# Kernel tuning notes

Measured on AMD Instinct MI355X. Metric: run time of the kernel, lower is better.

Reference implementation:

```python
import jax, jax.numpy as jnp
import numpy as np

B, S, D, H = 4, 2048, 2048, 16
DH = D // H


def setup_inputs() -> dict:
    key = jax.random.key(0)
    ks = jax.random.split(key, 11)
    p = 0.02  # keep pre-softmax logits in a sane range
    return {
        "x": jax.random.normal(ks[0], (B, S, D), jnp.float32),
        "Wq": jax.random.normal(ks[1], (D, D), jnp.float32) * p,
        "bq": jax.random.normal(ks[2], (D,), jnp.float32) * p,
        "Wk": jax.random.normal(ks[3], (D, D), jnp.float32) * p,
        "bk": jax.random.normal(ks[4], (D,), jnp.float32) * p,
        "Wv": jax.random.normal(ks[5], (D, D), jnp.float32) * p,
        "bv": jax.random.normal(ks[6], (D,), jnp.float32) * p,
        "Wo": jax.random.normal(ks[7], (D, D), jnp.float32) * p,
        "bo": jax.random.normal(ks[8], (D,), jnp.float32) * p,
        "spiral_weight": jax.random.normal(ks[9], (H,), jnp.float32),
        "helix_rotation": jax.random.normal(ks[10], (D,), jnp.float32),
    }


def reference(x, Wq, bq, Wk, bk, Wv, bv, Wo, bo, spiral_weight, helix_rotation):
    b, s, d = x.shape
    h, dh = H, d // H
    # projections (torch Linear: x @ W.T + b), split into heads
    q = (x @ Wq.T + bq).reshape(b, s, h, dh)
    k = (x @ Wk.T + bk).reshape(b, s, h, dh)
    v = (x @ Wv.T + bv).reshape(b, s, h, dh)
    # cos/sin helix gating, applied per (head, head_dim) channel
    rot = helix_rotation.reshape(h, dh)
    q = q * jnp.cos(rot)
    k = k * jnp.sin(rot)
    # per-head scaled scores: [b,h,s,s]
    scores = jnp.einsum("bshd,bthd->bhst", q, k) / np.sqrt(dh).astype(np.float32)
    scores = scores * spiral_weight[None, :, None, None]
    attn = jax.nn.softmax(scores, axis=-1)
    out = jnp.einsum("bhst,bthd->bshd", attn, v).reshape(b, s, d)
    return out @ Wo.T + bo
```

## Files before the change

kernel.cpp:

```cpp
#include <hip/hip_runtime.h>
#include <math.h>

#define B_ 4
#define S_ 2048
#define D_ 2048
#define H_ 16
#define DH_ 128

typedef unsigned short u16;
typedef unsigned int u32;
typedef u16 u16x8 __attribute__((ext_vector_type(8)));
typedef __bf16 bf16x8 __attribute__((ext_vector_type(8)));
typedef float f32x4 __attribute__((ext_vector_type(4)));

__device__ inline u16 f2bf(float f) {
    unsigned int u = __builtin_bit_cast(unsigned int, f);
    unsigned int lsb = (u >> 16) & 1u;
    u += 0x7fffu + lsb;
    return (u16)(u >> 16);
}

__device__ inline f32x4 mfma16(u16x8 a, u16x8 b, f32x4 c) {
    return __builtin_amdgcn_mfma_f32_16x16x32_bf16(
        __builtin_bit_cast(bf16x8, a), __builtin_bit_cast(bf16x8, b), c, 0, 0, 0);
}

__device__ inline void gl2lds16(const u16* g, u16* l) {
    __builtin_amdgcn_global_load_lds(
        (const __attribute__((address_space(1))) void*)g,
        (__attribute__((address_space(3))) void*)l, 16, 0, 0);
}

__device__ inline void block_barrier() {
    asm volatile("" ::: "memory");
    __builtin_amdgcn_s_barrier();
    asm volatile("" ::: "memory");
}

__global__ __launch_bounds__(256) void cvt_f32_bf16(const float* __restrict__ src,
                                                    u16* __restrict__ dst, int n8) {
    int i = blockIdx.x * 256 + threadIdx.x;
    if (i >= n8) return;
    const float4* s = (const float4*)src + (size_t)i * 2;
    float4 a = s[0], b = s[1];
    u16x8 o;
    o[0] = f2bf(a.x); o[1] = f2bf(a.y); o[2] = f2bf(a.z); o[3] = f2bf(a.w);
    o[4] = f2bf(b.x); o[5] = f2bf(b.y); o[6] = f2bf(b.z); o[7] = f2bf(b.w);
    *((u16x8*)dst + i) = o;
}

__global__ __launch_bounds__(256) void cvt4_f32_bf16(const float* __restrict__ s0,
                                                     const float* __restrict__ s1,
                                                     const float* __restrict__ s2,
                                                     const float* __restrict__ s3,
                                                     u16* __restrict__ dst) {
    const int region = blockIdx.x >> 11;
    const int i = (blockIdx.x & 2047) * 256 + threadIdx.x;
    const float* src = region == 0 ? s0 : region == 1 ? s1 : region == 2 ? s2 : s3;
    const float4* s = (const float4*)src + (size_t)i * 2;
    float4 a = s[0], b = s[1];
    u16x8 o;
    o[0] = f2bf(a.x); o[1] = f2bf(a.y); o[2] = f2bf(a.z); o[3] = f2bf(a.w);
    o[4] = f2bf(b.x); o[5] = f2bf(b.y); o[6] = f2bf(b.z); o[7] = f2bf(b.w);
    *((u16x8*)dst + (size_t)region * 524288 + i) = o;
}

template <int VOUT, typename OutT>
__device__ __forceinline__ void gemm_core(const u16* __restrict__ A,
                                          const u16* __restrict__ Bw,
                                          const float* __restrict__ bias,
                                          const float* __restrict__ helix,
                                          OutT* __restrict__ C,
                                          int M, int N, int K,
                                          int tm, int tn, int gate) {
    __shared__ __align__(16) u16 As[2][256 * 64];
    __shared__ __align__(16) u16 Bs[2][256 * 64];

    const int tid = threadIdx.x;
    const int lane = tid & 63, w = tid >> 6;
    const int lr = lane & 15, quad = lane >> 4;
    const int wm = w & 1, wn = w >> 1;
    const int NT = K >> 6;

    const u16* Asrc = A + (size_t)(tm * 256) * K;
    const u16* Bsrc = Bw + (size_t)(tn * 256) * K;

    u32 go[4][2];
    u32 lo[4][2];
#pragma unroll
    for (int q = 0; q < 2; ++q) {
        const int seg = w * 2 + q;
        const int i0 = seg * 8 + (lane >> 3);
        const int s0 = seg * 8;
        int row = (i0 & 63) | ((i0 >> 6) << 7);
        int rb = (s0 & 63) | ((s0 >> 6) << 7);
        go[0][q] = (u32)row * K + (((lane & 7) ^ (row & 7)) << 3);
        lo[0][q] = rb << 6;
        row += 64; rb += 64;
        go[3][q] = (u32)row * K + (((lane & 7) ^ (row & 7)) << 3);
        lo[3][q] = rb << 6;
        row = (i0 & 31) | ((i0 >> 5) << 6);
        rb = (s0 & 31) | ((s0 >> 5) << 6);
        go[1][q] = (u32)row * K + (((lane & 7) ^ (row & 7)) << 3);
        lo[1][q] = rb << 6;
        row += 32; rb += 32;
        go[2][q] = (u32)row * K + (((lane & 7) ^ (row & 7)) << 3);
        lo[2][q] = rb << 6;
    }

#define STAGE(u, tt)                                                          \
    do {                                                                      \
        const int kt_ = (((tt) < NT) ? (tt) : (NT - 1)) << 6;                 \
        const u16* gb_ = ((u) == 1 || (u) == 2) ? Bsrc : Asrc;                \
        u16* lb_ = ((u) == 1 || (u) == 2) ? Bs[(tt) & 1] : As[(tt) & 1];      \
        gl2lds16(gb_ + go[u][0] + kt_, lb_ + lo[u][0]);                       \
        gl2lds16(gb_ + go[u][1] + kt_, lb_ + lo[u][1]);                       \
    } while (0)

    const int koff0 = (quad * 8) ^ ((lr & 7) * 8);
    const int koff1 = (32 + quad * 8) ^ ((lr & 7) * 8);
    const int rA = wm * 128 + lr;
    const int rB = wn * 64 + lr;

    f32x4 zero = {0.f, 0.f, 0.f, 0.f};
    f32x4 acc[8][4];
#pragma unroll
    for (int im = 0; im < 8; ++im)
#pragma unroll
        for (int jn = 0; jn < 4; ++jn) acc[im][jn] = zero;

    u16x8 af[4][2], bf[4][2];

    STAGE(0, 0); STAGE(1, 0); STAGE(2, 0); STAGE(3, 0);
    STAGE(0, 1); STAGE(1, 1); STAGE(2, 1);
    asm volatile("s_waitcnt vmcnt(6)" ::: "memory");
    block_barrier();

    for (int t = 0; t < NT; ++t) {
        const u16* Ab = As[t & 1];
        const u16* Bb = Bs[t & 1];

#pragma unroll
        for (int im = 0; im < 4; ++im) {
            af[im][0] = *(const u16x8*)&Ab[(rA + im * 16) * 64 + koff0];
            af[im][1] = *(const u16x8*)&Ab[(rA + im * 16) * 64 + koff1];
        }
#pragma unroll
        for (int jn = 0; jn < 2; ++jn) {
            bf[jn][0] = *(const u16x8*)&Bb[(rB + jn * 16) * 64 + koff0];
            bf[jn][1] = *(const u16x8*)&Bb[(rB + jn * 16) * 64 + koff1];
        }
        STAGE(3, t + 1);
        block_barrier();
        asm volatile("s_waitcnt lgkmcnt(0)" ::: "memory");
        __builtin_amdgcn_s_setprio(1);
#pragma unroll
        for (int s = 0; s < 2; ++s)
#pragma unroll
            for (int im = 0; im < 4; ++im)
#pragma unroll
                for (int jn = 0; jn < 2; ++jn)
                    acc[im][jn] = mfma16(af[im][s], bf[jn][s], acc[im][jn]);
        __builtin_amdgcn_s_setprio(0);
        block_barrier();

#pragma unroll
        for (int jn = 2; jn < 4; ++jn) {
            bf[jn][0] = *(const u16x8*)&Bb[(rB + jn * 16) * 64 + koff0];
            bf[jn][1] = *(const u16x8*)&Bb[(rB + jn * 16) * 64 + koff1];
        }
        STAGE(0, t + 2);
        block_barrier();
        asm volatile("s_waitcnt lgkmcnt(0)" ::: "memory");
        __builtin_amdgcn_s_setprio(1);
#pragma unroll
        for (int s = 0; s < 2; ++s)
#pragma unroll
            for (int im = 0; im < 4; ++im)
#pragma unroll
                for (int jn = 2; jn < 4; ++jn)
                    acc[im][jn] = mfma16(af[im][s], bf[jn][s], acc[im][jn]);
        __builtin_amdgcn_s_setprio(0);
        block_barrier();

#pragma unroll
        for (int im = 0; im < 4; ++im) {
            af[im][0] = *(const u16x8*)&Ab[(rA + 64 + im * 16) * 64 + koff0];
            af[im][1] = *(const u16x8*)&Ab[(rA + 64 + im * 16) * 64 + koff1];
        }
        STAGE(1, t + 2);
        block_barrier();
        asm volatile("s_waitcnt lgkmcnt(0)" ::: "memory");
        __builtin_amdgcn_s_setprio(1);
#pragma unroll
        for (int s = 0; s < 2; ++s)
#pragma unroll
            for (int im = 0; im < 4; ++im)
#pragma unroll
                for (int jn = 0; jn < 2; ++jn)
                    acc[im + 4][jn] = mfma16(af[im][s], bf[jn][s], acc[im + 4][jn]);
        __builtin_amdgcn_s_setprio(0);
        block_barrier();

        STAGE(2, t + 2);
        asm volatile("s_waitcnt vmcnt(6)" ::: "memory");
        block_barrier();
        __builtin_amdgcn_s_setprio(1);
#pragma unroll
        for (int s = 0; s < 2; ++s)
#pragma unroll
            for (int im = 0; im < 4; ++im)
#pragma unroll
                for (int jn = 2; jn < 4; ++jn)
                    acc[im + 4][jn] = mfma16(af[im][s], bf[jn][s], acc[im + 4][jn]);
        __builtin_amdgcn_s_setprio(0);
        block_barrier();
    }
    asm volatile("s_waitcnt vmcnt(0)" ::: "memory");
#undef STAGE

    if constexpr (VOUT) {
#pragma unroll
        for (int im = 0; im < 8; ++im)
#pragma unroll
            for (int r = 0; r < 4; ++r) {
                int row = tm * 256 + wm * 128 + im * 16 + quad * 4 + r;
                float bs = bias[row];
#pragma unroll
                for (int jn = 0; jn < 4; ++jn) {
                    int col = tn * 256 + wn * 64 + jn * 16 + lr;
                    float val = acc[im][jn][r] + bs;
                    ((u16*)C)[(size_t)(col >> 11) * ((size_t)D_ * S_) +
                              (size_t)row * S_ + (col & (S_ - 1))] = f2bf(val);
                }
            }
    } else {
#pragma unroll
        for (int jn = 0; jn < 4; ++jn) {
            int col = tn * 256 + wn * 64 + jn * 16 + lr;
            float bs = bias[col];
            float g = 1.0f;
            if (gate == 1) g = cosf(helix[col]);
            if (gate == 2) g = sinf(helix[col]);
#pragma unroll
            for (int im = 0; im < 8; ++im)
#pragma unroll
                for (int r = 0; r < 4; ++r) {
                    int row = tm * 256 + wm * 128 + im * 16 + quad * 4 + r;
                    float val = (acc[im][jn][r] + bs) * g;
                    if constexpr (sizeof(OutT) == 2)
                        ((u16*)C)[(size_t)row * N + col] = f2bf(val);
                    else
                        ((float*)C)[(size_t)row * N + col] = val;
                }
        }
    }
}

template <int VOUT, typename OutT>
__global__ __launch_bounds__(512, 2) void gemm256(const u16* __restrict__ A,
                                                  const u16* __restrict__ Bw,
                                                  const float* __restrict__ bias,
                                                  const float* __restrict__ helix,
                                                  OutT* __restrict__ C,
                                                  int M, int N, int K, int gate) {
    gemm_core<VOUT, OutT>(A, Bw, bias, helix, C, M, N, K, blockIdx.y, blockIdx.x, gate);
}

__global__ __launch_bounds__(512, 2) void gemm256_qk(const u16* __restrict__ A,
                                                     const u16* __restrict__ Wq,
                                                     const u16* __restrict__ Wk,
                                                     const float* __restrict__ bq,
                                                     const float* __restrict__ bk,
                                                     const float* __restrict__ helix,
                                                     u16* __restrict__ Cq,
                                                     u16* __restrict__ Ck,
                                                     int M, int N, int K) {
    const int sel = blockIdx.x >> 3;
    const int tn = blockIdx.x & 7;
    gemm_core<0, u16>(A, sel ? Wk : Wq, sel ? bk : bq, helix, sel ? Ck : Cq,
                      M, N, K, blockIdx.y, tn, 1 + sel);
}

__global__ __launch_bounds__(256, 2) void helix_attn(const u16* __restrict__ Q,
                                                     const u16* __restrict__ Kq,
                                                     const u16* __restrict__ Vt,
                                                     const float* __restrict__ spiral,
                                                     u16* __restrict__ O) {
    __shared__ __align__(16) u16 Ks[64 * 128];
    __shared__ __align__(16) u16 Vs[128 * 72];
    __shared__ __align__(16) u16 Ps[128 * 72];

    const int tid = threadIdx.x;
    const int lane = tid & 63, w = tid >> 6;
    const int lr = lane & 15, quad = lane >> 4;

    const int bx = blockIdx.x;
    const int qt = bx & 15;
    const int h = (bx >> 4) & 15;
    const int b = bx >> 8;

    const size_t headoff = (size_t)b * S_ * D_ + (size_t)h * DH_;
    const u16* qp = Q + headoff;
    const u16* kp = Kq + headoff;
    const u16* vtp = Vt + ((size_t)b * H_ + h) * (size_t)DH_ * S_;

    const float scale2 = spiral[h] * 0.08838834764831845f * 1.4426950408889634f;

    u16x8 qf[2][4];
#pragma unroll
    for (int mb = 0; mb < 2; ++mb)
#pragma unroll
        for (int c = 0; c < 4; ++c) {
            u16x8 raw = *(const u16x8*)(qp + (size_t)(qt * 128 + mb * 64 + w * 16 + lr) * D_ +
                                        c * 32 + quad * 8);
#pragma unroll
            for (int j = 0; j < 8; ++j) {
                float f = __builtin_bit_cast(float, (u32)raw[j] << 16) * scale2;
                qf[mb][c][j] = f2bf(f);
            }
        }

    f32x4 zero = {0.f, 0.f, 0.f, 0.f};
    f32x4 Oacc[2][8];
#pragma unroll
    for (int mb = 0; mb < 2; ++mb)
#pragma unroll
        for (int n = 0; n < 8; ++n) Oacc[mb][n] = zero;
    float rs[2][4] = {{0.f, 0.f, 0.f, 0.f}, {0.f, 0.f, 0.f, 0.f}};

    const int rsw = (lr >> 1) & 7;
    const int wsw = (quad * 2) & 7;
    const int ksw = lr & 7;

    for (int tt = 0; tt < 32; ++tt) {
        const int t0 = tt * 64;
        __syncthreads();
#pragma unroll
        for (int p = 0; p < 4; ++p) {
            int lin = p * 256 + tid;
            int trow = lin >> 4;
            int kch = lin & 15;
            *(u16x8*)&Ks[trow * 128 + ((kch ^ (trow & 7)) * 8)] =
                *(const u16x8*)(kp + (size_t)(t0 + trow) * D_ + kch * 8);
            int drow = lin >> 3;
            int tch = (lin & 7) * 8;
            *(u16x8*)&Vs[drow * 72 + tch] =
                *(const u16x8*)(vtp + (size_t)drow * S_ + t0 + tch);
        }
        __syncthreads();

        f32x4 Sacc[2][4] = {{zero, zero, zero, zero}, {zero, zero, zero, zero}};
#pragma unroll
        for (int c = 0; c < 4; ++c) {
#pragma unroll
            for (int j = 0; j < 4; ++j) {
                u16x8 kf = *(const u16x8*)&Ks[(j * 16 + lr) * 128 +
                                              (((c * 4 + quad) ^ ksw) * 8)];
                Sacc[0][j] = mfma16(qf[0][c], kf, Sacc[0][j]);
                Sacc[1][j] = mfma16(qf[1][c], kf, Sacc[1][j]);
            }
        }

#pragma unroll
        for (int mb = 0; mb < 2; ++mb)
#pragma unroll
            for (int j = 0; j < 4; ++j)
#pragma unroll
                for (int r = 0; r < 4; ++r) {
                    float p = exp2f(Sacc[mb][j][r]);
                    u32 u = __builtin_bit_cast(u32, p);
                    rs[mb][r] += __builtin_bit_cast(float, u & 0xffff0000u);
                    int prow = mb * 64 + w * 16 + quad * 4 + r;
                    int pchunk = (j * 2 + (lr >> 3)) ^ ((wsw + (r >> 1)) & 7);
                    Ps[prow * 72 + pchunk * 8 + (lr & 7)] = (u16)(u >> 16);
                }

#pragma unroll
        for (int ks = 0; ks < 2; ++ks) {
            int pch = ((ks * 4 + quad) ^ rsw) * 8;
            u16x8 pf0 = *(const u16x8*)&Ps[(w * 16 + lr) * 72 + pch];
            u16x8 pf1 = *(const u16x8*)&Ps[(64 + w * 16 + lr) * 72 + pch];
#pragma unroll
            for (int n = 0; n < 8; ++n) {
                u16x8 vf = *(const u16x8*)&Vs[(n * 16 + lr) * 72 + ks * 32 + quad * 8];
                Oacc[0][n] = mfma16(pf0, vf, Oacc[0][n]);
                Oacc[1][n] = mfma16(pf1, vf, Oacc[1][n]);
            }
        }
    }

#pragma unroll
    for (int mb = 0; mb < 2; ++mb)
#pragma unroll
        for (int r = 0; r < 4; ++r) {
            float s = rs[mb][r];
#pragma unroll
            for (int off = 1; off < 16; off <<= 1) s += __shfl_xor(s, off, 64);
            float inv = 1.0f / s;
            int row = qt * 128 + mb * 64 + w * 16 + quad * 4 + r;
            u16* op = O + headoff + (size_t)row * D_;
#pragma unroll
            for (int n = 0; n < 8; ++n) op[n * 16 + lr] = f2bf(Oacc[mb][n][r] * inv);
        }
}

extern "C" void kernel_launch(void* const* d_in, const int* in_sizes, int n_in,
                              void* d_out, int out_size, void* d_ws, size_t ws_size,
                              hipStream_t stream) {
    const float* x = (const float*)d_in[0];
    const float* Wq = (const float*)d_in[1];
    const float* bq = (const float*)d_in[2];
    const float* Wk = (const float*)d_in[3];
    const float* bk = (const float*)d_in[4];
    const float* Wv = (const float*)d_in[5];
    const float* bv = (const float*)d_in[6];
    const float* Wo = (const float*)d_in[7];
    const float* bo = (const float*)d_in[8];
    const float* spiral = (const float*)d_in[9];
    const float* helix = (const float*)d_in[10];
    float* out = (float*)d_out;

    char* ws = (char*)d_ws;
    u16* xbf = (u16*)(ws);
    u16* wqb = (u16*)(ws + 33554432);
    u16* wkb = (u16*)(ws + 33554432 + 8388608);
    u16* wvb = (u16*)(ws + 33554432 + 16777216);
    u16* wob = (u16*)(ws + 33554432 + 25165824);
    u16* qb = (u16*)(ws + 67108864);
    u16* kb = (u16*)(ws + 67108864 + 33554432);
    u16* vtb = (u16*)(ws + 67108864 + 67108864);
    u16* attnb = xbf;

    const int NX = B_ * S_ * D_;

    cvt_f32_bf16<<<NX / 8 / 256, 256, 0, stream>>>(x, xbf, NX / 8);
    cvt4_f32_bf16<<<4 * 2048, 256, 0, stream>>>(Wq, Wk, Wv, Wo, wqb);

    dim3 gqk(2 * D_ / 256, (B_ * S_) / 256);
    gemm256_qk<<<gqk, 512, 0, stream>>>(xbf, wqb, wkb, bq, bk, helix, qb, kb,
                                        B_ * S_, D_, D_);
    dim3 gv((B_ * S_) / 256, D_ / 256);
    gemm256<1, u16><<<gv, 512, 0, stream>>>(wvb, xbf, bv, nullptr, vtb, D_, B_ * S_, D_, 0);

    helix_attn<<<B_ * H_ * (S_ / 128), 256, 0, stream>>>(qb, kb, vtb, spiral, attnb);

    dim3 gq(D_ / 256, (B_ * S_) / 256);
    gemm256<0, float><<<gq, 512, 0, stream>>>(attnb, wob, bo, nullptr, out, B_ * S_, D_, D_, 0);
}
```

Measured before the change: 674.6 us.

## Fuse Q/K/V projection GEMMs into one launch and swizzle attention V/P LDS

Merges the separate QK and V projection GEMM launches into a single 768-block kernel that picks operands, gate and output layout per block region. This removes one launch and the tail of the first GEMM, letting the V tiles fill idle CUs. In the attention kernel, the padded 72-element rows for V and P in shared memory become 64-element rows with an XOR swizzle, cutting LDS use while aiming to keep reads conflict-free. The runtime vout branch replaces a compile-time template, which could add register pressure or code size in the GEMM epilogue.

```diff
diff --git a/kernel.cpp b/kernel.cpp
--- a/kernel.cpp
+++ b/kernel.cpp
@@ -65,14 +65,14 @@
     *((u16x8*)dst + (size_t)region * 524288 + i) = o;
 }
 
-template <int VOUT, typename OutT>
+template <typename OutT>
 __device__ __forceinline__ void gemm_core(const u16* __restrict__ A,
                                           const u16* __restrict__ Bw,
                                           const float* __restrict__ bias,
                                           const float* __restrict__ helix,
                                           OutT* __restrict__ C,
-                                          int M, int N, int K,
-                                          int tm, int tn, int gate) {
+                                          int N, int K,
+                                          int tm, int tn, int gate, int vout) {
     __shared__ __align__(16) u16 As[2][256 * 64];
     __shared__ __align__(16) u16 Bs[2][256 * 64];
 
@@ -219,7 +219,7 @@
     asm volatile("s_waitcnt vmcnt(0)" ::: "memory");
 #undef STAGE
 
-    if constexpr (VOUT) {
+    if (vout) {
 #pragma unroll
         for (int im = 0; im < 8; ++im)
 #pragma unroll
@@ -257,29 +257,46 @@
     }
 }
 
-template <int VOUT, typename OutT>
+template <typename OutT>
 __global__ __launch_bounds__(512, 2) void gemm256(const u16* __restrict__ A,
                                                   const u16* __restrict__ Bw,
                                                   const float* __restrict__ bias,
                                                   const float* __restrict__ helix,
                                                   OutT* __restrict__ C,
-                                                  int M, int N, int K, int gate) {
-    gemm_core<VOUT, OutT>(A, Bw, bias, helix, C, M, N, K, blockIdx.y, blockIdx.x, gate);
-}
-
-__global__ __launch_bounds__(512, 2) void gemm256_qk(const u16* __restrict__ A,
-                                                     const u16* __restrict__ Wq,
-                                                     const u16* __restrict__ Wk,
-                                                     const float* __restrict__ bq,
-                                                     const float* __restrict__ bk,
-                                                     const float* __restrict__ helix,
-                                                     u16* __restrict__ Cq,
-                                                     u16* __restrict__ Ck,
-                                                     int M, int N, int K) {
-    const int sel = blockIdx.x >> 3;
-    const int tn = blockIdx.x & 7;
-    gemm_core<0, u16>(A, sel ? Wk : Wq, sel ? bk : bq, helix, sel ? Ck : Cq,
-                      M, N, K, blockIdx.y, tn, 1 + sel);
+                                                  int N, int K, int gate) {
+    gemm_core<OutT>(A, Bw, bias, helix, C, N, K, blockIdx.y, blockIdx.x, gate, 0);
+}
+
+__global__ __launch_bounds__(512, 2) void gemm256_qkv(const u16* __restrict__ xbf,
+                                                      const u16* __restrict__ Wq,
+                                                      const u16* __restrict__ Wk,
+                                                      const u16* __restrict__ Wv,
+                                                      const float* __restrict__ bq,
+                                                      const float* __restrict__ bk,
+                                                      const float* __restrict__ bv,
+                                                      const float* __restrict__ helix,
+                                                      u16* __restrict__ Cq,
+                                                      u16* __restrict__ Ck,
+                                                      u16* __restrict__ Cv) {
+    const int bid = blockIdx.x;
+    const int region = bid >> 8;
+    const int r = bid & 255;
+    const u16* A;
+    const u16* Bw;
+    const float* bias;
+    u16* C;
+    int tm, tn, gate, vout;
+    if (region == 0) {
+        A = xbf; Bw = Wq; bias = bq; C = Cq;
+        tn = r & 7; tm = r >> 3; gate = 1; vout = 0;
+    } else if (region == 1) {
+        A = xbf; Bw = Wk; bias = bk; C = Ck;
+        tn = r & 7; tm = r >> 3; gate = 2; vout = 0;
+    } else {
+        A = Wv; Bw = xbf; bias = bv; C = Cv;
+        tn = r & 31; tm = r >> 5; gate = 0; vout = 1;
+    }
+    gemm_core<u16>(A, Bw, bias, helix, C, D_, D_, tm, tn, gate, vout);
 }
 
 __global__ __launch_bounds__(256, 2) void helix_attn(const u16* __restrict__ Q,
@@ -288,8 +305,8 @@
                                                      const float* __restrict__ spiral,
                                                      u16* __restrict__ O) {
     __shared__ __align__(16) u16 Ks[64 * 128];
-    __shared__ __align__(16) u16 Vs[128 * 72];
-    __shared__ __align__(16) u16 Ps[128 * 72];
+    __shared__ __align__(16) u16 Vs[128 * 64];
+    __shared__ __align__(16) u16 Ps[128 * 64];
 
     const int tid = threadIdx.x;
     const int lane = tid & 63, w = tid >> 6;
@@ -344,9 +361,9 @@
             *(u16x8*)&Ks[trow * 128 + ((kch ^ (trow & 7)) * 8)] =
                 *(const u16x8*)(kp + (size_t)(t0 + trow) * D_ + kch * 8);
             int drow = lin >> 3;
-            int tch = (lin & 7) * 8;
-            *(u16x8*)&Vs[drow * 72 + tch] =
-                *(const u16x8*)(vtp + (size_t)drow * S_ + t0 + tch);
+            int lc = lin & 7;
+            *(u16x8*)&Vs[drow * 64 + ((lc ^ (drow & 7)) * 8)] =
+                *(const u16x8*)(vtp + (size_t)drow * S_ + t0 + lc * 8);
         }
         __syncthreads();
 
@@ -373,17 +390,18 @@
                     rs[mb][r] += __builtin_bit_cast(float, u & 0xffff0000u);
                     int prow = mb * 64 + w * 16 + quad * 4 + r;
                     int pchunk = (j * 2 + (lr >> 3)) ^ ((wsw + (r >> 1)) & 7);
-                    Ps[prow * 72 + pchunk * 8 + (lr & 7)] = (u16)(u >> 16);
+                    Ps[prow * 64 + pchunk * 8 + (lr & 7)] = (u16)(u >> 16);
                 }
 
 #pragma unroll
         for (int ks = 0; ks < 2; ++ks) {
             int pch = ((ks * 4 + quad) ^ rsw) * 8;
-            u16x8 pf0 = *(const u16x8*)&Ps[(w * 16 + lr) * 72 + pch];
-            u16x8 pf1 = *(const u16x8*)&Ps[(64 + w * 16 + lr) * 72 + pch];
+            u16x8 pf0 = *(const u16x8*)&Ps[(w * 16 + lr) * 64 + pch];
+            u16x8 pf1 = *(const u16x8*)&Ps[(64 + w * 16 + lr) * 64 + pch];
 #pragma unroll
             for (int n = 0; n < 8; ++n) {
-                u16x8 vf = *(const u16x8*)&Vs[(n * 16 + lr) * 72 + ks * 32 + quad * 8];
+                u16x8 vf = *(const u16x8*)&Vs[(n * 16 + lr) * 64 +
+                                              (((ks * 4 + quad) ^ ksw) * 8)];
                 Oacc[0][n] = mfma16(pf0, vf, Oacc[0][n]);
                 Oacc[1][n] = mfma16(pf1, vf, Oacc[1][n]);
             }
@@ -437,14 +455,11 @@
     cvt_f32_bf16<<<NX / 8 / 256, 256, 0, stream>>>(x, xbf, NX / 8);
     cvt4_f32_bf16<<<4 * 2048, 256, 0, stream>>>(Wq, Wk, Wv, Wo, wqb);
 
-    dim3 gqk(2 * D_ / 256, (B_ * S_) / 256);
-    gemm256_qk<<<gqk, 512, 0, stream>>>(xbf, wqb, wkb, bq, bk, helix, qb, kb,
-                                        B_ * S_, D_, D_);
-    dim3 gv((B_ * S_) / 256, D_ / 256);
-    gemm256<1, u16><<<gv, 512, 0, stream>>>(wvb, xbf, bv, nullptr, vtb, D_, B_ * S_, D_, 0);
+    gemm256_qkv<<<768, 512, 0, stream>>>(xbf, wqb, wkb, wvb, bq, bk, bv, helix,
+                                         qb, kb, vtb);
 
     helix_attn<<<B_ * H_ * (S_ / 128), 256, 0, stream>>>(qb, kb, vtb, spiral, attnb);
 
     dim3 gq(D_ / 256, (B_ * S_) / 256);
-    gemm256<0, float><<<gq, 512, 0, stream>>>(attnb, wob, bo, nullptr, out, B_ * S_, D_, D_, 0);
-}
+    gemm256<float><<<gq, 512, 0, stream>>>(attnb, wob, bo, nullptr, out, D_, D_, 0);
+}
```

After: 691.1 us. 1.02x slower.
